# Kernel optimization log

Measured on AMD Instinct MI355X. Metric: run time of the kernel, lower is better.

Reference implementation:

```python
import jax, jax.numpy as jnp
import numpy as np

EPS = 1e-5  # torch nn.LayerNorm default

def _ln(z, g, b):
    m = jnp.mean(z, axis=-1, keepdims=True)
    v = jnp.mean((z - m) ** 2, axis=-1, keepdims=True)
    return (z - m) * jax.lax.rsqrt(v + EPS) * g + b

def setup_inputs() -> dict:
    key = jax.random.key(0)
    ks = jax.random.split(key, 5)
    S, B, I, H = 2048, 1, 2048, 2048
    stdv = 1.0 / float(np.sqrt(H))
    u = lambda k, shape: jax.random.uniform(k, shape, jnp.float32, -stdv, stdv)
    return {
        "x": jax.random.normal(ks[0], (S, B, I), jnp.float32),
        "w_ih": u(ks[1], (4 * H, I)),
        "w_hh": u(ks[2], (4 * H, H)),
        "b_ih": u(ks[3], (4 * H,)),
        "b_hh": u(ks[4], (4 * H,)),
        # LN params for [input_gate, forget_gate, cell_gate, output_gate, cy]
        "ln_gamma": jnp.ones((5, H), jnp.float32),
        "ln_beta": jnp.zeros((5, H), jnp.float32),
    }

def reference(x, w_ih, w_hh, b_ih, b_hh, ln_gamma, ln_beta):
    S, B, I = x.shape
    H = w_hh.shape[1]
    # hoist the input projection out of the recurrence: one big GEMM
    xg = jnp.einsum('sbi,gi->sbg', x, w_ih) + b_ih + b_hh  # (S, B, 4H)
    h0 = jnp.zeros((B, H), x.dtype)
    c0 = jnp.zeros((B, H), x.dtype)

    def step(carry, xg_t):
        h, c = carry
        gates = xg_t + h @ w_hh.T                     # (B, 4H)
        i_, f_, g_, o_ = jnp.split(gates, 4, axis=-1)
        i = jax.nn.sigmoid(_ln(i_, ln_gamma[0], ln_beta[0]))
        f = jax.nn.sigmoid(_ln(f_, ln_gamma[1], ln_beta[1]))
        g = jnp.tanh(_ln(g_, ln_gamma[2], ln_beta[2]))
        o = jax.nn.sigmoid(_ln(o_, ln_gamma[3], ln_beta[3]))
        cy = _ln(f * c + i * g, ln_gamma[4], ln_beta[4])
        hy = o * jnp.tanh(cy)
        return (hy, cy), hy

    (hy, cy), hs = jax.lax.scan(step, (h0, c0), xg)   # hs: (S, B, H)
    # torch: y = stack([h[-1] for h in ht]).unsqueeze(1) -> last batch row, (S,1,H)
    y = hs[:, -1, :][:, None, :]
    return y, hy, cy
```

## Files before the change

kernel.cpp:

```cpp
#include <hip/hip_runtime.h>

typedef float f32x2 __attribute__((ext_vector_type(2)));
typedef float f32x4 __attribute__((ext_vector_type(4)));
typedef short bf16x8 __attribute__((ext_vector_type(8)));
typedef _Float16 f16x2 __attribute__((ext_vector_type(2)));
typedef _Float16 f16x4 __attribute__((ext_vector_type(4)));
typedef _Float16 f16x8 __attribute__((ext_vector_type(8)));

#define SEQ 2048
#define HD 2048
#define NG 8192
#define KD 2048
#define NB 256
#define NT 512
#define PAD_CH 136

__device__ __forceinline__ unsigned short f32_to_bf16_rne(float f) {
    unsigned int u = __float_as_uint(f);
    u += 0x7FFFu + ((u >> 16) & 1u);
    return (unsigned short)(u >> 16);
}

__global__ void cvt_f16_kernel(const float* __restrict__ in, _Float16* __restrict__ out, int n) {
    for (int i = blockIdx.x * blockDim.x + threadIdx.x; i < n; i += gridDim.x * blockDim.x)
        out[i] = (_Float16)in[i];
}

__global__ __launch_bounds__(256) void gemm_xg(
    const float* __restrict__ A,
    const float* __restrict__ B,
    const float* __restrict__ bih, const float* __restrict__ bhh,
    float* __restrict__ C)
{
    __shared__ unsigned short As[128 * 32];
    __shared__ unsigned short Bs[128 * 32];
    const int tid = threadIdx.x;
    const int bm = blockIdx.x, bn = blockIdx.y;
    const int wave = tid >> 6, lane = tid & 63;
    const int wr = wave >> 1, wc = wave & 1;
    const int l15 = lane & 15, l4 = lane >> 4;

    f32x4 acc[4][4];
    #pragma unroll
    for (int i = 0; i < 4; ++i)
        #pragma unroll
        for (int j = 0; j < 4; ++j) {
            f32x4 z = {0.f, 0.f, 0.f, 0.f};
            acc[i][j] = z;
        }

    for (int k0 = 0; k0 < KD; k0 += 32) {
        #pragma unroll
        for (int i = 0; i < 2; ++i) {
            int idx = tid + i * 256;
            int row = idx >> 2, c8 = idx & 3;
            const float* ga = A + (size_t)(bm * 128 + row) * KD + k0 + c8 * 8;
            float4 a0 = *(const float4*)ga;
            float4 a1 = *(const float4*)(ga + 4);
            bf16x8 av;
            av[0] = (short)f32_to_bf16_rne(a0.x); av[1] = (short)f32_to_bf16_rne(a0.y);
            av[2] = (short)f32_to_bf16_rne(a0.z); av[3] = (short)f32_to_bf16_rne(a0.w);
            av[4] = (short)f32_to_bf16_rne(a1.x); av[5] = (short)f32_to_bf16_rne(a1.y);
            av[6] = (short)f32_to_bf16_rne(a1.z); av[7] = (short)f32_to_bf16_rne(a1.w);
            *(bf16x8*)&As[row * 32 + c8 * 8] = av;
            const float* gb = B + (size_t)(bn * 128 + row) * KD + k0 + c8 * 8;
            float4 b0 = *(const float4*)gb;
            float4 b1 = *(const float4*)(gb + 4);
            bf16x8 bv;
            bv[0] = (short)f32_to_bf16_rne(b0.x); bv[1] = (short)f32_to_bf16_rne(b0.y);
            bv[2] = (short)f32_to_bf16_rne(b0.z); bv[3] = (short)f32_to_bf16_rne(b0.w);
            bv[4] = (short)f32_to_bf16_rne(b1.x); bv[5] = (short)f32_to_bf16_rne(b1.y);
            bv[6] = (short)f32_to_bf16_rne(b1.z); bv[7] = (short)f32_to_bf16_rne(b1.w);
            *(bf16x8*)&Bs[row * 32 + c8 * 8] = bv;
        }
        __syncthreads();
        bf16x8 af[4], bfr[4];
        #pragma unroll
        for (int m = 0; m < 4; ++m) af[m] = *(const bf16x8*)&As[(wr * 64 + m * 16 + l15) * 32 + l4 * 8];
        #pragma unroll
        for (int n = 0; n < 4; ++n) bfr[n] = *(const bf16x8*)&Bs[(wc * 64 + n * 16 + l15) * 32 + l4 * 8];
        #pragma unroll
        for (int m = 0; m < 4; ++m)
            #pragma unroll
            for (int n = 0; n < 4; ++n)
                acc[m][n] = __builtin_amdgcn_mfma_f32_16x16x32_bf16(af[m], bfr[n], acc[m][n], 0, 0, 0);
        __syncthreads();
    }
    #pragma unroll
    for (int m = 0; m < 4; ++m) {
        #pragma unroll
        for (int n = 0; n < 4; ++n) {
            int col = bn * 128 + wc * 64 + n * 16 + l15;
            float bias = bih[col] + bhh[col];
            int row0 = bm * 128 + wr * 64 + m * 16 + l4 * 4;
            #pragma unroll
            for (int r = 0; r < 4; ++r)
                C[(size_t)(row0 + r) * NG + col] = acc[m][n][r] + bias;
        }
    }
}

__device__ __forceinline__ void st_llc16(float* p, f32x4 v) {
    asm volatile("global_store_dwordx4 %0, %1, off sc0 sc1" :: "v"(p), "v"(v) : "memory");
}
__device__ __forceinline__ void st_llc8(float* p, f32x2 v) {
    asm volatile("global_store_dwordx2 %0, %1, off sc0 sc1" :: "v"(p), "v"(v) : "memory");
}
__device__ __forceinline__ void ld_llc_issue_p(const float* p, f32x4& a, f32x4& b, f32x4& c, f32x4& d) {
    asm volatile(
        "global_load_dwordx4 %0, %4, off sc0 sc1\n\t"
        "global_load_dwordx4 %1, %4, off offset:16 sc0 sc1\n\t"
        "global_load_dwordx4 %2, %4, off offset:32 sc0 sc1\n\t"
        "global_load_dwordx4 %3, %4, off offset:48 sc0 sc1"
        : "=&v"(a), "=&v"(b), "=&v"(c), "=&v"(d)
        : "v"(p)
        : "memory");
}
__device__ __forceinline__ void ld_llc_issue4(const float* p0, const float* p1,
                                              const float* p2, const float* p3,
                                              f32x4& a, f32x4& b, f32x4& c, f32x4& d) {
    asm volatile(
        "global_load_dwordx4 %0, %4, off sc0 sc1\n\t"
        "global_load_dwordx4 %1, %5, off sc0 sc1\n\t"
        "global_load_dwordx4 %2, %6, off sc0 sc1\n\t"
        "global_load_dwordx4 %3, %7, off sc0 sc1"
        : "=&v"(a), "=&v"(b), "=&v"(c), "=&v"(d)
        : "v"(p0), "v"(p1), "v"(p2), "v"(p3)
        : "memory");
}
__device__ __forceinline__ void ld_gl16(const float* p, f32x4& a) {
    asm volatile("global_load_dwordx4 %0, %1, off" : "=&v"(a) : "v"(p) : "memory");
}
__device__ __forceinline__ void wait_vm5(f32x4& a, f32x4& b, f32x4& c, f32x4& d) {
    asm volatile("s_waitcnt vmcnt(5)" : "+v"(a), "+v"(b), "+v"(c), "+v"(d) :: "memory");
    __builtin_amdgcn_sched_barrier(0);
}
__device__ __forceinline__ void wait_vm1(f32x4& a, f32x4& b, f32x4& c, f32x4& d) {
    asm volatile("s_waitcnt vmcnt(1)" : "+v"(a), "+v"(b), "+v"(c), "+v"(d) :: "memory");
    __builtin_amdgcn_sched_barrier(0);
}
__device__ __forceinline__ void wait_vm0_1(f32x4& a) {
    asm volatile("s_waitcnt vmcnt(0)" : "+v"(a) :: "memory");
    __builtin_amdgcn_sched_barrier(0);
}

__device__ __forceinline__ float rcpf(float x) { return __builtin_amdgcn_rcpf(x); }
__device__ __forceinline__ float rsqf(float x) { return __builtin_amdgcn_rsqf(x); }
__device__ __forceinline__ float sigf(float x) { return rcpf(1.0f + __expf(-x)); }
__device__ __forceinline__ float tanhfast(float x) {
    float ax = fabsf(x);
    float e = __expf(-2.0f * ax);
    return __builtin_copysignf((1.0f - e) * rcpf(1.0f + e), x);
}

__device__ __forceinline__ void bar_lgkm() {
    asm volatile("s_waitcnt lgkmcnt(0)" ::: "memory");
    __builtin_amdgcn_s_barrier();
}
__device__ __forceinline__ void bar_full() {
    asm volatile("s_waitcnt vmcnt(0) lgkmcnt(0)" ::: "memory");
    __builtin_amdgcn_s_barrier();
}

#define DONE_OFF (8 * 64)

__global__ __launch_bounds__(512, 2) void lstm_rec(
    const float* __restrict__ xg,
    const _Float16* __restrict__ Whh,
    const float* __restrict__ gamma,
    const float* __restrict__ beta,
    float* __restrict__ gates,
    float* __restrict__ partials,
    unsigned* __restrict__ barctl,
    float* __restrict__ yout)
{
    __shared__ _Float16 hlds[16 * PAD_CH];
    __shared__ __align__(16) float red2[16];
    __shared__ __align__(16) float statsmem[8];

    const int b = blockIdx.x;
    const int t = threadIdx.x;
    const int wave = t >> 6, lane = t & 63;
    const int p = t * 4;

    unsigned* grpcnt = barctl + (b >> 5) * 64;

    const int row = t >> 4, sub = t & 15;
    const int grow = b * 32 + row;

    f16x8 wreg[16];
    {
        const _Float16* wsrc = Whh + (size_t)grow * HD + sub * 128;
        #pragma unroll
        for (int i = 0; i < 16; ++i) wreg[i] = *(const f16x8*)(wsrc + i * 8);
    }
    for (int k = t; k < 16 * PAD_CH; k += NT) hlds[k] = (_Float16)0.0f;

    float4 gm[4], bt[4];
    #pragma unroll
    for (int g = 0; g < 4; ++g) {
        gm[g] = *(const float4*)&gamma[g * HD + p];
        bt[g] = *(const float4*)&beta[g * HD + p];
    }
    float4 gm4 = *(const float4*)&gamma[4 * HD + p];
    float4 bt4 = *(const float4*)&beta[4 * HD + p];

    float* hyout = yout + (size_t)SEQ * HD;
    float* cyout = hyout + HD;
    const float invH = 1.0f / 2048.0f;

    float cprev[4] = {0.f, 0.f, 0.f, 0.f};

    f32x4 xg4 = {0.f, 0.f, 0.f, 0.f};
    if (lane == 0) xg4 = *(const f32x4*)(xg + b * 32 + wave * 4);

    const _Float16* hch = hlds + sub * PAD_CH;
    __syncthreads();

    for (int step = 0; step < SEQ; ++step) {
        float* gb = gates + (size_t)(step & 1) * NG;
        float* pb = partials + (size_t)(step & 1) * (NB * 8 * 2);
        const unsigned gen = (unsigned)(step + 1);

        float accv[4] = {0.f, 0.f, 0.f, 0.f};
        #pragma unroll
        for (int i = 0; i < 16; ++i) {
            f16x8 hv = *(const f16x8*)(hch + i * 8);
            const f16x2* w2 = (const f16x2*)&wreg[i];
            const f16x2* h2 = (const f16x2*)&hv;
            float x = accv[i & 3];
            x = __builtin_amdgcn_fdot2(w2[0], h2[0], x, false);
            x = __builtin_amdgcn_fdot2(w2[1], h2[1], x, false);
            x = __builtin_amdgcn_fdot2(w2[2], h2[2], x, false);
            x = __builtin_amdgcn_fdot2(w2[3], h2[3], x, false);
            accv[i & 3] = x;
        }
        float r = (accv[0] + accv[1]) + (accv[2] + accv[3]);
        #pragma unroll
        for (int off = 1; off < 16; off <<= 1) r += __shfl_xor(r, off);
        float r1 = __shfl(r, 16), r2 = __shfl(r, 32), r3 = __shfl(r, 48);
        wait_vm0_1(xg4);
        if (lane == 0) {
            float g0 = r + xg4[0], g1 = r1 + xg4[1], g2 = r2 + xg4[2], g3 = r3 + xg4[3];
            f32x4 gv4 = {g0, g1, g2, g3};
            st_llc16(&gb[b * 32 + wave * 4], gv4);
            f32x2 pq = {(g0 + g1) + (g2 + g3),
                        (g0 * g0 + g1 * g1) + (g2 * g2 + g3 * g3)};
            st_llc8(&pb[(b * 8 + wave) * 2], pq);
        }

        bar_full();

        if (t == 0) {
            asm volatile("" ::: "memory");
            unsigned o1 = __hip_atomic_fetch_add(grpcnt, 1u, __ATOMIC_RELAXED, __HIP_MEMORY_SCOPE_AGENT);
            if (o1 == gen * 32u - 1u)
                __hip_atomic_store(barctl + DONE_OFF + (b >> 5) * 64, gen,
                                   __ATOMIC_RELAXED, __HIP_MEMORY_SCOPE_AGENT);
        }
        for (;;) {
            unsigned v = 0xFFFFFFFFu;
            if (lane < 8)
                v = __hip_atomic_load(barctl + DONE_OFF + lane * 64, __ATOMIC_RELAXED, __HIP_MEMORY_SCOPE_AGENT);
            if (__all(v >= gen)) break;
            __builtin_amdgcn_s_sleep(1);
        }
        asm volatile("" ::: "memory");

        f32x4 pa, pbv, pc, pd;
        if (wave < 4)
            ld_llc_issue_p(&pb[wave * 1024 + lane * 16], pa, pbv, pc, pd);
        f32x4 gq[4];
        ld_llc_issue4(&gb[0 * HD + p], &gb[1 * HD + p], &gb[2 * HD + p], &gb[3 * HD + p],
                      gq[0], gq[1], gq[2], gq[3]);
        if (lane == 0 && step + 1 < SEQ)
            ld_gl16(xg + (size_t)(step + 1) * NG + b * 32 + wave * 4, xg4);

        if (wave < 4) {
            wait_vm5(pa, pbv, pc, pd);
            float s = ((pa[0] + pa[2]) + (pbv[0] + pbv[2])) + ((pc[0] + pc[2]) + (pd[0] + pd[2]));
            float q = ((pa[1] + pa[3]) + (pbv[1] + pbv[3])) + ((pc[1] + pc[3]) + (pd[1] + pd[3]));
            #pragma unroll
            for (int off = 1; off < 64; off <<= 1) { s += __shfl_xor(s, off); q += __shfl_xor(q, off); }
            if (lane == 0) {
                float m = s * invH;
                statsmem[wave * 2] = m;
                statsmem[wave * 2 + 1] = rsqf(q * invH - m * m + 1e-5f);
            }
        }
        bar_lgkm();

        wait_vm1(gq[0], gq[1], gq[2], gq[3]);
        float mg[4], rg[4];
        {
            const f32x4* sm = (const f32x4*)statsmem;
            f32x4 s0 = sm[0], s1 = sm[1];
            mg[0] = s0[0]; rg[0] = s0[1]; mg[1] = s0[2]; rg[1] = s0[3];
            mg[2] = s1[0]; rg[2] = s1[1]; mg[3] = s1[2]; rg[3] = s1[3];
        }

        float rcv[4], og4[4];
        float s2 = 0.f, q2 = 0.f;
        #pragma unroll
        for (int j = 0; j < 4; ++j) {
            float li = (gq[0][j] - mg[0]) * rg[0] * ((const float*)&gm[0])[j] + ((const float*)&bt[0])[j];
            float lf = (gq[1][j] - mg[1]) * rg[1] * ((const float*)&gm[1])[j] + ((const float*)&bt[1])[j];
            float lg = (gq[2][j] - mg[2]) * rg[2] * ((const float*)&gm[2])[j] + ((const float*)&bt[2])[j];
            float lo = (gq[3][j] - mg[3]) * rg[3] * ((const float*)&gm[3])[j] + ((const float*)&bt[3])[j];
            float ig = sigf(li);
            float fg = sigf(lf);
            float gg = tanhfast(lg);
            float og = sigf(lo);
            float rv = fg * cprev[j] + ig * gg;
            rcv[j] = rv; og4[j] = og;
            s2 += rv; q2 += rv * rv;
        }
        #pragma unroll
        for (int off = 1; off < 64; off <<= 1) { s2 += __shfl_xor(s2, off); q2 += __shfl_xor(q2, off); }
        if (lane == 0) { red2[wave] = s2; red2[8 + wave] = q2; }
        bar_lgkm();

        float mc, rc;
        {
            const f32x4* r4 = (const f32x4*)red2;
            f32x4 sa = r4[0], sb = r4[1], qa = r4[2], qb = r4[3];
            float s = ((sa[0] + sa[1]) + (sa[2] + sa[3])) + ((sb[0] + sb[1]) + (sb[2] + sb[3]));
            float q = ((qa[0] + qa[1]) + (qa[2] + qa[3])) + ((qb[0] + qb[1]) + (qb[2] + qb[3]));
            mc = s * invH;
            rc = rsqf(q * invH - mc * mc + 1e-5f);
        }

        float hvf[4], lcf[4];
        f16x4 hh;
        #pragma unroll
        for (int j = 0; j < 4; ++j) {
            float lc = (rcv[j] - mc) * rc * ((const float*)&gm4)[j] + ((const float*)&bt4)[j];
            cprev[j] = lc;
            float th = tanhfast(lc);
            float hv = og4[j] * th;
            hvf[j] = hv; lcf[j] = lc;
            hh[j] = (_Float16)hv;
        }
        *(f16x4*)&hlds[(t >> 5) * PAD_CH + (p & 127)] = hh;

        if ((t >> 1) == b) {
            float4 ho = {hvf[0], hvf[1], hvf[2], hvf[3]};
            *(float4*)&yout[(size_t)step * HD + p] = ho;
            if (step == SEQ - 1) {
                *(float4*)&hyout[p] = ho;
                float4 co = {lcf[0], lcf[1], lcf[2], lcf[3]};
                *(float4*)&cyout[p] = co;
            }
        }
        bar_lgkm();
    }
}

extern "C" void kernel_launch(void* const* d_in, const int* in_sizes, int n_in,
                              void* d_out, int out_size, void* d_ws, size_t ws_size,
                              hipStream_t stream) {
    const float* x   = (const float*)d_in[0];
    const float* wih = (const float*)d_in[1];
    const float* whh = (const float*)d_in[2];
    const float* bih = (const float*)d_in[3];
    const float* bhh = (const float*)d_in[4];
    const float* gam = (const float*)d_in[5];
    const float* bet = (const float*)d_in[6];
    float* out = (float*)d_out;

    char* ws = (char*)d_ws;
    size_t off = 0;
    auto carve = [&](size_t bytes) -> void* {
        void* pp = ws + off;
        off += (bytes + 255) & ~(size_t)255;
        return pp;
    };
    float* xg      = (float*)carve(sizeof(float) * (size_t)SEQ * NG);
    _Float16* whhf = (_Float16*)carve(sizeof(_Float16) * (size_t)NG * HD);
    float* gates   = (float*)carve(sizeof(float) * 2 * NG);
    float* parts   = (float*)carve(sizeof(float) * 2 * NB * 8 * 2);
    unsigned* barctl = (unsigned*)carve(sizeof(unsigned) * 16 * 64);

    cvt_f16_kernel<<<2048, 256, 0, stream>>>(whh, whhf, NG * HD);
    dim3 ggrid(16, 64);
    gemm_xg<<<ggrid, 256, 0, stream>>>(x, wih, bih, bhh, xg);
    hipMemsetAsync(barctl, 0, sizeof(unsigned) * 16 * 64, stream);

    void* args[] = { (void*)&xg, (void*)&whhf, (void*)&gam, (void*)&bet,
                     (void*)&gates, (void*)&parts, (void*)&barctl, (void*)&out };
    hipLaunchCooperativeKernel((void*)lstm_rec, dim3(NB), dim3(NT), args, 0, stream);
}
```

Before: 9.958 ms.

## Replace block barrier plus per-block arrive with per-wave arrival counters across 64 lines

Each wave now arrives at the grid barrier on its own, so the intra-block s_barrier with vmcnt drain before arrival is gone. Arrival counters are spread over 64 cache lines of 32 waves each, and all 64 lanes poll the done flags. The y output store is deferred to after the next barrier, so it no longer sits on the path before the arrival, and the xg prefetch wait moves to the top of the step. This cuts per-step critical-path latency but puts more atomic and polling traffic on the L2.

```diff
diff --git a/kernel.cpp b/kernel.cpp
--- a/kernel.cpp
+++ b/kernel.cpp
@@ -157,12 +157,8 @@
     asm volatile("s_waitcnt lgkmcnt(0)" ::: "memory");
     __builtin_amdgcn_s_barrier();
 }
-__device__ __forceinline__ void bar_full() {
-    asm volatile("s_waitcnt vmcnt(0) lgkmcnt(0)" ::: "memory");
-    __builtin_amdgcn_s_barrier();
-}
-
-#define DONE_OFF (8 * 64)
+
+#define DONE_OFF (64 * 64)
 
 __global__ __launch_bounds__(512, 2) void lstm_rec(
     const float* __restrict__ xg,
@@ -183,10 +179,12 @@
     const int wave = t >> 6, lane = t & 63;
     const int p = t * 4;
 
-    unsigned* grpcnt = barctl + (b >> 5) * 64;
+    const int wline = (b * 8 + wave) >> 5;
+    unsigned* arrcnt = barctl + wline * 64;
 
     const int row = t >> 4, sub = t & 15;
     const int grow = b * 32 + row;
+    const bool owner = ((t >> 1) == b);
 
     f16x8 wreg[16];
     {
@@ -210,6 +208,8 @@
     const float invH = 1.0f / 2048.0f;
 
     float cprev[4] = {0.f, 0.f, 0.f, 0.f};
+    float4 prevy = {0.f, 0.f, 0.f, 0.f};
+    float4 prevc = {0.f, 0.f, 0.f, 0.f};
 
     f32x4 xg4 = {0.f, 0.f, 0.f, 0.f};
     if (lane == 0) xg4 = *(const f32x4*)(xg + b * 32 + wave * 4);
@@ -221,6 +221,8 @@
         float* gb = gates + (size_t)(step & 1) * NG;
         float* pb = partials + (size_t)(step & 1) * (NB * 8 * 2);
         const unsigned gen = (unsigned)(step + 1);
+
+        wait_vm0_1(xg4);
 
         float accv[4] = {0.f, 0.f, 0.f, 0.f};
         #pragma unroll
@@ -239,7 +241,6 @@
         #pragma unroll
         for (int off = 1; off < 16; off <<= 1) r += __shfl_xor(r, off);
         float r1 = __shfl(r, 16), r2 = __shfl(r, 32), r3 = __shfl(r, 48);
-        wait_vm0_1(xg4);
         if (lane == 0) {
             float g0 = r + xg4[0], g1 = r1 + xg4[1], g2 = r2 + xg4[2], g3 = r3 + xg4[3];
             f32x4 gv4 = {g0, g1, g2, g3};
@@ -249,23 +250,23 @@
             st_llc8(&pb[(b * 8 + wave) * 2], pq);
         }
 
-        bar_full();
-
-        if (t == 0) {
-            asm volatile("" ::: "memory");
-            unsigned o1 = __hip_atomic_fetch_add(grpcnt, 1u, __ATOMIC_RELAXED, __HIP_MEMORY_SCOPE_AGENT);
+        asm volatile("s_waitcnt vmcnt(0)" ::: "memory");
+        if (lane == 0) {
+            unsigned o1 = __hip_atomic_fetch_add(arrcnt, 1u, __ATOMIC_RELAXED, __HIP_MEMORY_SCOPE_AGENT);
             if (o1 == gen * 32u - 1u)
-                __hip_atomic_store(barctl + DONE_OFF + (b >> 5) * 64, gen,
+                __hip_atomic_store(barctl + DONE_OFF + wline * 64, gen,
                                    __ATOMIC_RELAXED, __HIP_MEMORY_SCOPE_AGENT);
         }
         for (;;) {
-            unsigned v = 0xFFFFFFFFu;
-            if (lane < 8)
-                v = __hip_atomic_load(barctl + DONE_OFF + lane * 64, __ATOMIC_RELAXED, __HIP_MEMORY_SCOPE_AGENT);
+            unsigned v = __hip_atomic_load(barctl + DONE_OFF + lane * 64,
+                                           __ATOMIC_RELAXED, __HIP_MEMORY_SCOPE_AGENT);
             if (__all(v >= gen)) break;
             __builtin_amdgcn_s_sleep(1);
         }
         asm volatile("" ::: "memory");
+
+        if (step > 0 && owner)
+            *(float4*)&yout[(size_t)(step - 1) * HD + p] = prevy;
 
         f32x4 pa, pbv, pc, pd;
         if (wave < 4)
@@ -273,8 +274,8 @@
         f32x4 gq[4];
         ld_llc_issue4(&gb[0 * HD + p], &gb[1 * HD + p], &gb[2 * HD + p], &gb[3 * HD + p],
                       gq[0], gq[1], gq[2], gq[3]);
-        if (lane == 0 && step + 1 < SEQ)
-            ld_gl16(xg + (size_t)(step + 1) * NG + b * 32 + wave * 4, xg4);
+        if (lane == 0)
+            ld_gl16(xg + (size_t)((step + 1) & (SEQ - 1)) * NG + b * 32 + wave * 4, xg4);
 
         if (wave < 4) {
             wait_vm5(pa, pbv, pc, pd);
@@ -330,7 +331,6 @@
             rc = rsqf(q * invH - mc * mc + 1e-5f);
         }
 
-        float hvf[4], lcf[4];
         f16x4 hh;
         #pragma unroll
         for (int j = 0; j < 4; ++j) {
@@ -338,21 +338,18 @@
             cprev[j] = lc;
             float th = tanhfast(lc);
             float hv = og4[j] * th;
-            hvf[j] = hv; lcf[j] = lc;
+            ((float*)&prevy)[j] = hv;
+            ((float*)&prevc)[j] = lc;
             hh[j] = (_Float16)hv;
         }
         *(f16x4*)&hlds[(t >> 5) * PAD_CH + (p & 127)] = hh;
-
-        if ((t >> 1) == b) {
-            float4 ho = {hvf[0], hvf[1], hvf[2], hvf[3]};
-            *(float4*)&yout[(size_t)step * HD + p] = ho;
-            if (step == SEQ - 1) {
-                *(float4*)&hyout[p] = ho;
-                float4 co = {lcf[0], lcf[1], lcf[2], lcf[3]};
-                *(float4*)&cyout[p] = co;
-            }
-        }
         bar_lgkm();
+    }
+
+    if (owner) {
+        *(float4*)&yout[(size_t)(SEQ - 1) * HD + p] = prevy;
+        *(float4*)&hyout[p] = prevy;
+        *(float4*)&cyout[p] = prevc;
     }
 }
 
@@ -379,12 +376,12 @@
     _Float16* whhf = (_Float16*)carve(sizeof(_Float16) * (size_t)NG * HD);
     float* gates   = (float*)carve(sizeof(float) * 2 * NG);
     float* parts   = (float*)carve(sizeof(float) * 2 * NB * 8 * 2);
-    unsigned* barctl = (unsigned*)carve(sizeof(unsigned) * 16 * 64);
+    unsigned* barctl = (unsigned*)carve(sizeof(unsigned) * 128 * 64);
 
     cvt_f16_kernel<<<2048, 256, 0, stream>>>(whh, whhf, NG * HD);
     dim3 ggrid(16, 64);
     gemm_xg<<<ggrid, 256, 0, stream>>>(x, wih, bih, bhh, xg);
-    hipMemsetAsync(barctl, 0, sizeof(unsigned) * 16 * 64, stream);
+    hipMemsetAsync(barctl, 0, sizeof(unsigned) * 128 * 64, stream);
 
     void* args[] = { (void*)&xg, (void*)&whhf, (void*)&gam, (void*)&bet,
                      (void*)&gates, (void*)&parts, (void*)&barctl, (void*)&out };
```

New measurement: 12.75 ms. 1.28x slower.
